# Kernel tuning notes

Hardware: AMD Instinct MI355X
Metric: run time of the kernel (lower is better)

Reference implementation:

```python
import jax, jax.numpy as jnp
import numpy as np

LAMBDA_VIOLATION = 0.5
NUM_SAMPLES = 128
EPS = 1e-09
B = 4096
K_MAX = 128
NK_MAX = 128
# unique (n, k, m) parameter combos, cycled over the batch
COMBOS = np.array([[256, 128, 3], [192, 96, 3], [224, 112, 4], [160, 80, 2]], dtype=np.int64)


def setup_inputs() -> dict:
    key = jax.random.key(0)
    k1, k2, k3 = jax.random.split(key, 3)
    y_pred = jax.random.uniform(k1, (B, 1), minval=0.5, maxval=8.0, dtype=jnp.float32)
    y_true = jax.random.uniform(k2, (B, 1), minval=0.5, maxval=8.0, dtype=jnp.float32)
    P_padded = jax.random.normal(k3, (B, K_MAX, NK_MAX), dtype=jnp.float32)
    params = jnp.asarray(COMBOS[np.arange(B) % len(COMBOS)])  # [B, 3] int64
    return {"y_pred": y_pred, "y_true": y_true, "P_padded": P_padded, "params": params}


def reference(y_pred, y_true, P_padded, params):
    # LogMSE in base 2
    log2_pred = jnp.log2(jnp.clip(y_pred, EPS))
    log2_true = jnp.log2(jnp.clip(y_true, EPS))
    loss_logmse = jnp.mean((log2_true - log2_pred) ** 2)

    batch = P_padded.shape[0]
    p_np = np.asarray(params)  # int params are concrete constants
    combos, inverse = np.unique(p_np, axis=0, return_inverse=True)

    total_penalty = jnp.asarray(0.0, dtype=y_pred.dtype)
    xkey = jax.random.key(42)
    for i in range(combos.shape[0]):
        n, k, m = int(combos[i, 0]), int(combos[i, 1]), int(combos[i, 2])
        idx = np.nonzero(inverse == i)[0]
        if m + 1 > n or k <= 0 or n - k < 0 or idx.size == 0:
            continue
        g = idx.size
        P_actual = P_padded[idx, :k, : n - k]            # [g, k, n-k]
        X = jax.random.normal(jax.random.fold_in(xkey, i), (g, NUM_SAMPLES, k), dtype=y_pred.dtype)
        # G = [I_k | P_actual]  =>  C = X @ G = [X | X @ P_actual]
        C = jnp.concatenate([X, jnp.einsum('bsk,bkp->bsp', X, P_actual)], axis=2)  # [g, S, n]
        mags = jnp.abs(C)
        top, _ = jax.lax.top_k(mags, m + 1)              # [g, S, m+1] sorted descending
        hm = top[..., 0] / (top[..., m] + EPS)           # c_max / c_m
        max_hm = jnp.max(hm, axis=1)                     # [g]
        penalty = jax.nn.relu(max_hm - y_pred[idx].squeeze(-1))
        total_penalty = total_penalty + jnp.sum(penalty)

    loss_violation = total_penalty / batch
    total_loss = loss_logmse + LAMBDA_VIOLATION * loss_violation
    return total_loss, loss_logmse, loss_violation
```

## Files before the change

kernel.cpp:

```cpp
#include <hip/hip_runtime.h>
#include <stdint.h>

typedef short bf16x8 __attribute__((ext_vector_type(8)));
typedef float f32x4 __attribute__((ext_vector_type(4)));

__host__ __device__ inline uint32_t rotl32(uint32_t v, int d) {
  return (v << d) | (v >> (32 - d));
}

__host__ __device__ inline void tf2x32(uint32_t k0, uint32_t k1,
                                       uint32_t x0, uint32_t x1,
                                       uint32_t& o0, uint32_t& o1) {
  uint32_t ks0 = k0, ks1 = k1, ks2 = k0 ^ k1 ^ 0x1BD11BDAu;
  x0 += ks0; x1 += ks1;
#define TF_R(r) { x0 += x1; x1 = rotl32(x1, (r)); x1 ^= x0; }
  TF_R(13) TF_R(15) TF_R(26) TF_R(6)
  x0 += ks1; x1 += ks2 + 1u;
  TF_R(17) TF_R(29) TF_R(16) TF_R(24)
  x0 += ks2; x1 += ks0 + 2u;
  TF_R(13) TF_R(15) TF_R(26) TF_R(6)
  x0 += ks0; x1 += ks1 + 3u;
  TF_R(17) TF_R(29) TF_R(16) TF_R(24)
  x0 += ks1; x1 += ks2 + 4u;
  TF_R(13) TF_R(15) TF_R(26) TF_R(6)
  x0 += ks2; x1 += ks0 + 5u;
#undef TF_R
  o0 = x0; o1 = x1;
}

__device__ __forceinline__ float erfinv_xla(float x) {
  float w = -__logf(fmaf(-x, x, 1.0f));
  float p;
  if (w < 5.0f) {
    w = w - 2.5f;
    p = 2.81022636e-08f;
    p = fmaf(p, w, 3.43273939e-07f);
    p = fmaf(p, w, -3.5233877e-06f);
    p = fmaf(p, w, -4.39150654e-06f);
    p = fmaf(p, w, 0.00021858087f);
    p = fmaf(p, w, -0.00125372503f);
    p = fmaf(p, w, -0.00417768164f);
    p = fmaf(p, w, 0.246640727f);
    p = fmaf(p, w, 1.50140941f);
  } else {
    w = sqrtf(w) - 3.0f;
    p = -0.000200214257f;
    p = fmaf(p, w, 0.000100950558f);
    p = fmaf(p, w, 0.00134934322f);
    p = fmaf(p, w, -0.00367342844f);
    p = fmaf(p, w, 0.00573950773f);
    p = fmaf(p, w, -0.0076224613f);
    p = fmaf(p, w, 0.00943887047f);
    p = fmaf(p, w, 1.00167406f);
    p = fmaf(p, w, 2.83297682f);
  }
  return p * x;
}

__device__ __forceinline__ float bits_to_normal(uint32_t bits) {
  uint32_t fb = (bits >> 9) | 0x3F800000u;
  float f = __uint_as_float(fb) - 1.0f;
  const float lo = -0.99999994f;
  float u = fmaf(f, 1.0f - lo, lo);
  u = fmaxf(lo, u);
  return 1.41421356f * erfinv_xla(u);
}

__device__ __forceinline__ uint32_t f2bf(float x) {
  uint32_t b = __float_as_uint(x);
  return (b + 0x7FFFu + ((b >> 16) & 1u)) >> 16;
}
__device__ __forceinline__ float bf2f_s(short h) {
  return __uint_as_float(((uint32_t)(uint16_t)h) << 16);
}

__device__ __forceinline__ bf16x8 pack8(const float (&r)[8]) {
  union { bf16x8 v; uint32_t u[4]; } o;
#pragma unroll
  for (int p = 0; p < 4; ++p)
    o.u[p] = f2bf(r[2 * p]) | (f2bf(r[2 * p + 1]) << 16);
  return o.v;
}

template <int T>
__device__ __forceinline__ void insT(float (&t)[T], float v) {
  if constexpr (T == 1) {
    t[0] = fmaxf(t[0], v);
  } else {
    float t0o = t[0], t1o = t[1];
    t[0] = fmaxf(t0o, v);
    t[1] = __builtin_amdgcn_fmed3f(v, t0o, t1o);
    float a = fminf(fminf(v, t0o), t1o);
#pragma unroll
    for (int q = 2; q < T; ++q) {
      float tq = t[q];
      t[q] = fmaxf(tq, a);
      a = fminf(tq, a);
    }
  }
}

template <int K, int KP, int T>
__device__ void process_combo(const float* __restrict__ Pp,
                              const float* __restrict__ yp,
                              const float* __restrict__ yt,
                              float* __restrict__ accum,
                              int ofs, uint32_t key0, uint32_t key1,
                              int rp, char* sm) {
  constexpr int KSTEPS = KP / 32;
  constexpr int NCH = (K + 31) / 32;
  constexpr int PH = K / 2;
  constexpr int ITERS = PH / 4;
  constexpr int XSTR = KP + 8;
  constexpr int XSTRU = XSTR / 2;
  constexpr int XROW_U = 64 * XSTRU;
  constexpr int REGION = 2 * 64 * XSTR * 2;
  constexpr bool SKIP1 = (K % 32) == 16;
  constexpr uint32_t HALF = 65536u * (uint32_t)K;

  const int tid = threadIdx.x;
  const int wave = tid >> 6;
  const int lane = tid & 63;
  const int quad = lane >> 4;
  const int l15 = lane & 15;
  const int row = wave >> 1;
  const int msub = (wave & 1) * 32;

  const int b0 = 4 * rp + ofs;
  const int b1 = 4 * (rp + 512) + ofs;

  uint32_t* Xu = (uint32_t*)sm;
  float* Xpool = (float*)(sm + REGION);
  float* wvmax = Xpool + 128 * T;
  float* maxhm = wvmax + 4;

  if (tid < 2) maxhm[tid] = 0.0f;

  const float* Pr = Pp + (size_t)(row ? b1 : b0) * 16384 + quad * (8 * 128) + l15;

  for (int pass = 0; pass < 2; ++pass) {
#pragma unroll
    for (int it = 0; it < ITERS; ++it) {
      int q = it * 256 + tid;
      int s_loc = q / PH;
      int k = 2 * (q - s_loc * PH);
      uint32_t ctr = (uint32_t)((rp * 128 + pass * 64 + s_loc) * K + k);
      uint32_t o0a, o1a, o0b, o1b;
      tf2x32(key0, key1, ctr, ctr + HALF, o0a, o1a);
      tf2x32(key0, key1, ctr + 1u, ctr + 1u + HALF, o0b, o1b);
      uint32_t idx = (uint32_t)(s_loc * XSTRU + (k >> 1));
      uint32_t h0 = f2bf(bits_to_normal(o0a));
      uint32_t h1 = f2bf(bits_to_normal(o0b));
      Xu[idx] = h0 | (h1 << 16);
      h0 = f2bf(bits_to_normal(o1a));
      h1 = f2bf(bits_to_normal(o1b));
      Xu[XROW_U + idx] = h0 | (h1 << 16);
    }
    if constexpr (KP > K) {
      constexpr int PADU = (KP - K) / 2;
      for (int p = tid; p < 2 * 64 * PADU; p += 256) {
        int rs = p / PADU;
        int r = p - rs * PADU;
        Xu[rs * XSTRU + K / 2 + r] = 0;
      }
    }
    __syncthreads();

    bf16x8 ahi[2][KSTEPS];
#pragma unroll
    for (int f = 0; f < 2; ++f)
#pragma unroll
      for (int ks = 0; ks < KSTEPS; ++ks) {
        int off = ((row * 64 + msub + f * 16 + l15) * XSTR + ks * 32 + quad * 8) * 2;
        ahi[f][ks] = *(const bf16x8*)(sm + off);
      }
    {
      float t5x[2][T];
#pragma unroll
      for (int f = 0; f < 2; ++f) {
#pragma unroll
        for (int q = 0; q < T; ++q) t5x[f][q] = 0.0f;
#pragma unroll
        for (int ks = 0; ks < KSTEPS; ++ks)
#pragma unroll
          for (int j = 0; j < 8; ++j)
            insT(t5x[f], fabsf(bf2f_s(ahi[f][ks][j])));
      }
#pragma unroll
      for (int f = 0; f < 2; ++f) {
#pragma unroll
        for (int msk = 16; msk <= 32; msk <<= 1) {
          float o[T];
#pragma unroll
          for (int q = 0; q < T; ++q) o[q] = __shfl_xor(t5x[f][q], msk);
#pragma unroll
          for (int q = 0; q < T; ++q) insT(t5x[f], o[q]);
        }
      }
      if (lane < 16) {
#pragma unroll
        for (int f = 0; f < 2; ++f) {
          int slot = row * 64 + msub + f * 16 + l15;
#pragma unroll
          for (int q = 0; q < T; ++q) Xpool[slot * T + q] = t5x[f][q];
        }
      }
    }

    float t5y[2][4][T];
#pragma unroll
    for (int f = 0; f < 2; ++f)
#pragma unroll
      for (int r = 0; r < 4; ++r)
#pragma unroll
        for (int q = 0; q < T; ++q) t5y[f][r][q] = 0.0f;

#pragma unroll 1
    for (int c = 0; c < NCH; ++c) {
      const bool skip1 = SKIP1 && (c == NCH - 1);
      const float* bpc = Pr + c * 32;
      f32x4 acc[2][2];
#pragma unroll
      for (int f = 0; f < 2; ++f)
#pragma unroll
        for (int nf = 0; nf < 2; ++nf) acc[f][nf] = (f32x4){0.f, 0.f, 0.f, 0.f};

#pragma unroll
      for (int ks = 0; ks < KSTEPS; ++ks) {
        const float* bpk = bpc + ks * (32 * 128);
        {
          float r0[8];
#pragma unroll
          for (int j = 0; j < 8; ++j) r0[j] = bpk[j * 128];
          bf16x8 bh0 = pack8(r0);
#pragma unroll
          for (int f = 0; f < 2; ++f)
            acc[f][0] = __builtin_amdgcn_mfma_f32_16x16x32_bf16(ahi[f][ks], bh0, acc[f][0], 0, 0, 0);
        }
        if (!skip1) {
          float r1[8];
#pragma unroll
          for (int j = 0; j < 8; ++j) r1[j] = bpk[j * 128 + 16];
          bf16x8 bh1 = pack8(r1);
#pragma unroll
          for (int f = 0; f < 2; ++f)
            acc[f][1] = __builtin_amdgcn_mfma_f32_16x16x32_bf16(ahi[f][ks], bh1, acc[f][1], 0, 0, 0);
        }
      }
#pragma unroll
      for (int f = 0; f < 2; ++f)
#pragma unroll
        for (int r = 0; r < 4; ++r) {
          insT(t5y[f][r], fabsf(acc[f][0][r]));
          if (!skip1) insT(t5y[f][r], fabsf(acc[f][1][r]));
        }
    }

    float wmax = 0.0f;
#pragma unroll
    for (int f = 0; f < 2; ++f)
#pragma unroll
      for (int r = 0; r < 4; ++r) {
#pragma unroll
        for (int msk = 1; msk <= 8; msk <<= 1) {
          float o[T];
#pragma unroll
          for (int q = 0; q < T; ++q) o[q] = __shfl_xor(t5y[f][r][q], msk);
#pragma unroll
          for (int q = 0; q < T; ++q) insT(t5y[f][r], o[q]);
        }
        int slot = row * 64 + msub + f * 16 + quad * 4 + r;
        const float* xp = Xpool + slot * T;
#pragma unroll
        for (int q = 0; q < T; ++q) insT(t5y[f][r], xp[q]);
        float hm = t5y[f][r][0] / (t5y[f][r][T - 1] + 1e-9f);
        wmax = fmaxf(wmax, hm);
      }
    wmax = fmaxf(wmax, __shfl_xor(wmax, 16));
    wmax = fmaxf(wmax, __shfl_xor(wmax, 32));
    if (lane == 0) wvmax[wave] = wmax;
    __syncthreads();
    if (tid < 2)
      maxhm[tid] = fmaxf(maxhm[tid], fmaxf(wvmax[2 * tid], wvmax[2 * tid + 1]));
  }

  if (tid == 0) {
    float pen = fmaxf(maxhm[0] - yp[b0], 0.0f) + fmaxf(maxhm[1] - yp[b1], 0.0f);
    atomicAdd(&accum[0], pen);
    float d0 = log2f(fmaxf(yt[b0], 1e-9f)) - log2f(fmaxf(yp[b0], 1e-9f));
    float d1 = log2f(fmaxf(yt[b1], 1e-9f)) - log2f(fmaxf(yp[b1], 1e-9f));
    atomicAdd(&accum[1], fmaf(d0, d0, d1 * d1));
  }
}

struct ComboArgs {
  int ofs[4];
  uint32_t k0[4];
  uint32_t k1[4];
};

#define SM_BYTES (34816 + 2560 + 16 + 8)

__global__ __launch_bounds__(256, 2)
void viol_kernel(const float* __restrict__ Pp, const float* __restrict__ yp,
                 const float* __restrict__ yt, float* __restrict__ accum,
                 ComboArgs ca) {
  __shared__ __align__(16) char sm[SM_BYTES];
  int i = blockIdx.x >> 9;
  int rp = blockIdx.x & 511;
  switch (i) {
    case 0: process_combo< 80,  96, 3>(Pp, yp, yt, accum, ca.ofs[0], ca.k0[0], ca.k1[0], rp, sm); break;
    case 1: process_combo< 96,  96, 4>(Pp, yp, yt, accum, ca.ofs[1], ca.k0[1], ca.k1[1], rp, sm); break;
    case 2: process_combo<112, 128, 5>(Pp, yp, yt, accum, ca.ofs[2], ca.k0[2], ca.k1[2], rp, sm); break;
    default: process_combo<128, 128, 4>(Pp, yp, yt, accum, ca.ofs[3], ca.k0[3], ca.k1[3], rp, sm); break;
  }
}

__global__ void finalize_kernel(const float* __restrict__ accum, float* __restrict__ out) {
  if (threadIdx.x == 0 && blockIdx.x == 0) {
    float viol = accum[0] / 4096.0f;
    float lm = accum[1] / 4096.0f;
    out[0] = fmaf(0.5f, viol, lm);
    out[1] = lm;
    out[2] = viol;
  }
}

extern "C" void kernel_launch(void* const* d_in, const int* in_sizes, int n_in,
                              void* d_out, int out_size, void* d_ws, size_t ws_size,
                              hipStream_t stream) {
  const float* y_pred   = (const float*)d_in[0];
  const float* y_true   = (const float*)d_in[1];
  const float* P_padded = (const float*)d_in[2];
  float* accum = (float*)d_ws;
  float* out = (float*)d_out;

  hipMemsetAsync(accum, 0, 2 * sizeof(float), stream);

  ComboArgs ca;
  const int ofs[4] = {3, 1, 2, 0};
  for (int i = 0; i < 4; ++i) {
    ca.ofs[i] = ofs[i];
    uint32_t o0, o1;
    tf2x32(0u, 42u, 0u, (uint32_t)i, o0, o1);
    ca.k0[i] = o0;
    ca.k1[i] = o1;
  }

  viol_kernel<<<2048, 256, 0, stream>>>(P_padded, y_pred, y_true, accum, ca);
  finalize_kernel<<<1, 64, 0, stream>>>(accum, out);
}
```

Before: 488.4 us.

## Transpose MFMA operands so each lane owns a sample row; use hardware bf16 pack

New measurement: 461.8 us. 1.06x faster.

```diff
diff --git a/kernel.cpp b/kernel.cpp
--- a/kernel.cpp
+++ b/kernel.cpp
@@ -66,10 +66,12 @@
   return 1.41421356f * erfinv_xla(u);
 }
 
-__device__ __forceinline__ uint32_t f2bf(float x) {
-  uint32_t b = __float_as_uint(x);
-  return (b + 0x7FFFu + ((b >> 16) & 1u)) >> 16;
-}
+__device__ __forceinline__ uint32_t cvt_pk_bf16(float lo, float hi) {
+  uint32_t r;
+  asm("v_cvt_pk_bf16_f32 %0, %1, %2" : "=v"(r) : "v"(lo), "v"(hi));
+  return r;
+}
+
 __device__ __forceinline__ float bf2f_s(short h) {
   return __uint_as_float(((uint32_t)(uint16_t)h) << 16);
 }
@@ -78,7 +80,7 @@
   union { bf16x8 v; uint32_t u[4]; } o;
 #pragma unroll
   for (int p = 0; p < 4; ++p)
-    o.u[p] = f2bf(r[2 * p]) | (f2bf(r[2 * p + 1]) << 16);
+    o.u[p] = cvt_pk_bf16(r[2 * p], r[2 * p + 1]);
   return o.v;
 }
 
@@ -130,8 +132,7 @@
   const int b1 = 4 * (rp + 512) + ofs;
 
   uint32_t* Xu = (uint32_t*)sm;
-  float* Xpool = (float*)(sm + REGION);
-  float* wvmax = Xpool + 128 * T;
+  float* wvmax = (float*)(sm + REGION);
   float* maxhm = wvmax + 4;
 
   if (tid < 2) maxhm[tid] = 0.0f;
@@ -149,12 +150,8 @@
       tf2x32(key0, key1, ctr, ctr + HALF, o0a, o1a);
       tf2x32(key0, key1, ctr + 1u, ctr + 1u + HALF, o0b, o1b);
       uint32_t idx = (uint32_t)(s_loc * XSTRU + (k >> 1));
-      uint32_t h0 = f2bf(bits_to_normal(o0a));
-      uint32_t h1 = f2bf(bits_to_normal(o0b));
-      Xu[idx] = h0 | (h1 << 16);
-      h0 = f2bf(bits_to_normal(o1a));
-      h1 = f2bf(bits_to_normal(o1b));
-      Xu[XROW_U + idx] = h0 | (h1 << 16);
+      Xu[idx]          = cvt_pk_bf16(bits_to_normal(o0a), bits_to_normal(o0b));
+      Xu[XROW_U + idx] = cvt_pk_bf16(bits_to_normal(o1a), bits_to_normal(o1b));
     }
     if constexpr (KP > K) {
       constexpr int PADU = (KP - K) / 2;
@@ -174,46 +171,23 @@
         int off = ((row * 64 + msub + f * 16 + l15) * XSTR + ks * 32 + quad * 8) * 2;
         ahi[f][ks] = *(const bf16x8*)(sm + off);
       }
-    {
-      float t5x[2][T];
-#pragma unroll
-      for (int f = 0; f < 2; ++f) {
-#pragma unroll
-        for (int q = 0; q < T; ++q) t5x[f][q] = 0.0f;
-#pragma unroll
-        for (int ks = 0; ks < KSTEPS; ++ks)
-#pragma unroll
-          for (int j = 0; j < 8; ++j)
-            insT(t5x[f], fabsf(bf2f_s(ahi[f][ks][j])));
-      }
-#pragma unroll
-      for (int f = 0; f < 2; ++f) {
-#pragma unroll
-        for (int msk = 16; msk <= 32; msk <<= 1) {
-          float o[T];
-#pragma unroll
-          for (int q = 0; q < T; ++q) o[q] = __shfl_xor(t5x[f][q], msk);
-#pragma unroll
-          for (int q = 0; q < T; ++q) insT(t5x[f], o[q]);
-        }
-      }
-      if (lane < 16) {
-#pragma unroll
-        for (int f = 0; f < 2; ++f) {
-          int slot = row * 64 + msub + f * 16 + l15;
-#pragma unroll
-          for (int q = 0; q < T; ++q) Xpool[slot * T + q] = t5x[f][q];
-        }
-      }
-    }
-
-    float t5y[2][4][T];
+    float t5x[2][T];
+#pragma unroll
+    for (int f = 0; f < 2; ++f) {
+#pragma unroll
+      for (int q = 0; q < T; ++q) t5x[f][q] = 0.0f;
+#pragma unroll
+      for (int ks = 0; ks < KSTEPS; ++ks)
+#pragma unroll
+        for (int j = 0; j < 8; ++j)
+          insT(t5x[f], fabsf(bf2f_s(ahi[f][ks][j])));
+    }
+
+    float t5y[2][T];
 #pragma unroll
     for (int f = 0; f < 2; ++f)
 #pragma unroll
-      for (int r = 0; r < 4; ++r)
-#pragma unroll
-        for (int q = 0; q < T; ++q) t5y[f][r][q] = 0.0f;
+      for (int q = 0; q < T; ++q) t5y[f][q] = 0.0f;
 
 #pragma unroll 1
     for (int c = 0; c < NCH; ++c) {
@@ -235,7 +209,7 @@
           bf16x8 bh0 = pack8(r0);
 #pragma unroll
           for (int f = 0; f < 2; ++f)
-            acc[f][0] = __builtin_amdgcn_mfma_f32_16x16x32_bf16(ahi[f][ks], bh0, acc[f][0], 0, 0, 0);
+            acc[f][0] = __builtin_amdgcn_mfma_f32_16x16x32_bf16(bh0, ahi[f][ks], acc[f][0], 0, 0, 0);
         }
         if (!skip1) {
           float r1[8];
@@ -244,40 +218,37 @@
           bf16x8 bh1 = pack8(r1);
 #pragma unroll
           for (int f = 0; f < 2; ++f)
-            acc[f][1] = __builtin_amdgcn_mfma_f32_16x16x32_bf16(ahi[f][ks], bh1, acc[f][1], 0, 0, 0);
+            acc[f][1] = __builtin_amdgcn_mfma_f32_16x16x32_bf16(bh1, ahi[f][ks], acc[f][1], 0, 0, 0);
         }
       }
 #pragma unroll
       for (int f = 0; f < 2; ++f)
 #pragma unroll
         for (int r = 0; r < 4; ++r) {
-          insT(t5y[f][r], fabsf(acc[f][0][r]));
-          if (!skip1) insT(t5y[f][r], fabsf(acc[f][1][r]));
+          insT(t5y[f], fabsf(acc[f][0][r]));
+          if (!skip1) insT(t5y[f], fabsf(acc[f][1][r]));
         }
     }
 
     float wmax = 0.0f;
 #pragma unroll
-    for (int f = 0; f < 2; ++f)
-#pragma unroll
-      for (int r = 0; r < 4; ++r) {
-#pragma unroll
-        for (int msk = 1; msk <= 8; msk <<= 1) {
-          float o[T];
-#pragma unroll
-          for (int q = 0; q < T; ++q) o[q] = __shfl_xor(t5y[f][r][q], msk);
-#pragma unroll
-          for (int q = 0; q < T; ++q) insT(t5y[f][r], o[q]);
-        }
-        int slot = row * 64 + msub + f * 16 + quad * 4 + r;
-        const float* xp = Xpool + slot * T;
-#pragma unroll
-        for (int q = 0; q < T; ++q) insT(t5y[f][r], xp[q]);
-        float hm = t5y[f][r][0] / (t5y[f][r][T - 1] + 1e-9f);
-        wmax = fmaxf(wmax, hm);
+    for (int f = 0; f < 2; ++f) {
+#pragma unroll
+      for (int q = 0; q < T; ++q) insT(t5y[f], t5x[f][q]);
+#pragma unroll
+      for (int msk = 16; msk <= 32; msk <<= 1) {
+        float o[T];
+#pragma unroll
+        for (int q = 0; q < T; ++q) o[q] = __shfl_xor(t5y[f][q], msk);
+#pragma unroll
+        for (int q = 0; q < T; ++q) insT(t5y[f], o[q]);
       }
-    wmax = fmaxf(wmax, __shfl_xor(wmax, 16));
-    wmax = fmaxf(wmax, __shfl_xor(wmax, 32));
+      float hm = t5y[f][0] / (t5y[f][T - 1] + 1e-9f);
+      wmax = fmaxf(wmax, hm);
+    }
+#pragma unroll
+    for (int msk = 1; msk <= 8; msk <<= 1)
+      wmax = fmaxf(wmax, __shfl_xor(wmax, msk));
     if (lane == 0) wvmax[wave] = wmax;
     __syncthreads();
     if (tid < 2)
@@ -299,7 +270,7 @@
   uint32_t k1[4];
 };
 
-#define SM_BYTES (34816 + 2560 + 16 + 8)
+#define SM_BYTES (34816 + 16 + 8)
 
 __global__ __launch_bounds__(256, 2)
 void viol_kernel(const float* __restrict__ Pp, const float* __restrict__ yp,
```
